# Performance work log

Hardware: AMD Instinct MI355X
Metric: run time of the kernel (lower is better)

## Reference

```python
import jax, jax.numpy as jnp
import numpy as np

B = 1048576   # batch of samples
L = 81        # leaf classes (hardcoded in the module)
G = 9         # synthetic 2-level hierarchy: 9 groups of 9 leaves under one root


def setup_inputs() -> dict:
    key = jax.random.key(0)
    k1, k2 = jax.random.split(key)
    outputs = jax.random.normal(k1, (B, L), dtype=jnp.float32)
    target = jax.random.randint(k2, (B,), 0, L, dtype=jnp.int32)
    return {"outputs": outputs, "target": target}


def reference(outputs, target):
    sft = jax.nn.softmax(outputs, axis=1)                 # [B, 81] leaf probs
    gp = sft.reshape(-1, G, G).sum(-1)                    # [B, 9] internal-node probs (sum of descendant leaves)
    parent = target // G                                  # [B] parent group of each target leaf
    p_parent = jnp.take_along_axis(gp, parent[:, None], axis=1)[:, 0]
    p_leaf = jnp.take_along_axis(sft, target[:, None], axis=1)[:, 0]
    win = 0.5 * p_parent + 0.5 * p_leaf
    loss = -jnp.log(win).mean()
    # greedy top-down argmax prediction: best group, then best leaf within that group
    g = jnp.argmax(gp, axis=1)                            # [B]
    within = jnp.take_along_axis(sft.reshape(-1, G, G), g[:, None, None], axis=1)[:, 0, :]  # [B, 9]
    pred = g * G + jnp.argmax(within, axis=1)             # [B]
    # synchronized walk to common ancestor: leaves at equal depth -> dist in {0,1,2}
    same_group = (pred // G) == parent
    total_dist = jnp.where(pred == target, 0, jnp.where(same_group, 1, 2)).sum()
    return loss, pred, total_dist
```

## Files before the change

kernel.cpp:

```cpp
#include <hip/hip_runtime.h>
#include <cstdint>

constexpr int BTOT = 1048576;
constexpr int LCLS = 81;
constexpr int GRP  = 9;
constexpr int ROWS = 64;
constexpr int THR  = 64;
constexpr int NBLK = BTOT / ROWS;
constexpr int TILE4 = ROWS * LCLS / 4;
constexpr int FULLR = TILE4 / THR;
constexpr int TAIL  = TILE4 - FULLR * THR;
constexpr float FIX = 67108864.0f;

__device__ inline void gload_lds16(const float* gsrc, float* ldst) {
    __builtin_amdgcn_global_load_lds(
        (const __attribute__((address_space(1))) void*)gsrc,
        (__attribute__((address_space(3))) void*)ldst,
        16, 0, 0);
}

__device__ __attribute__((noinline)) int refine_group_f64(const float* __restrict__ xrow)
{
    double best = -1.0; int bi = 0;
    #pragma unroll
    for (int g = 0; g < GRP; ++g) {
        double s = 0.0;
        #pragma unroll
        for (int j = 0; j < GRP; ++j) s += exp((double)xrow[g * GRP + j]);
        if (s > best) { best = s; bi = g; }
    }
    return bi;
}

__global__ __launch_bounds__(THR) void hl_main(
    const float* __restrict__ x, const int* __restrict__ tgt,
    float* __restrict__ out, unsigned long long* __restrict__ part)
{
    __shared__ float tile[ROWS * LCLS];
    const int tid = threadIdx.x;
    const size_t tbase = (size_t)blockIdx.x * (ROWS * LCLS);
    const float* gt = x + tbase;

    #pragma unroll
    for (int r = 0; r < FULLR; ++r) {
        const int i = r * THR + tid;
        gload_lds16(gt + 4 * i, &tile[4 * i]);
    }
    if (tid < TAIL) {
        const int i = FULLR * THR + tid;
        gload_lds16(gt + 4 * i, &tile[4 * i]);
    }
    __syncthreads();

    const int row = blockIdx.x * ROWS + tid;
    const float* xr = tile + tid * LCLS;

    float gs[GRP];
    #pragma unroll
    for (int g = 0; g < GRP; ++g) {
        float s = 0.0f;
        #pragma unroll
        for (int j = 0; j < GRP; ++j) s += __expf(xr[g * GRP + j]);
        gs[g] = s;
    }
    float S = gs[0];
    #pragma unroll
    for (int g = 1; g < GRP; ++g) S += gs[g];

    float g1 = gs[0], g2 = -1e30f; int gi = 0;
    #pragma unroll
    for (int g = 1; g < GRP; ++g) {
        float v = gs[g];
        bool gt2 = v > g1;
        g2 = gt2 ? g1 : (v > g2 ? v : g2);
        g1 = gt2 ? v  : g1;
        gi = gt2 ? g  : gi;
    }

    const int t = tgt[row];
    const int parent = t / GRP;

    float gpar = gs[0];
    #pragma unroll
    for (int g = 1; g < GRP; ++g)
        gpar = (parent == g) ? gs[g] : gpar;

    if (g1 - g2 < 1e-5f * g1) gi = refine_group_f64(xr);

    const int wb = gi * GRP;
    float w1 = xr[wb]; int wi = 0;
    #pragma unroll
    for (int j = 1; j < GRP; ++j) {
        float v = xr[wb + j];
        if (v > w1) { w1 = v; wi = j; }
    }

    const int pred = gi * GRP + wi;

    float et  = expf(xr[t]);
    float win = 0.5f * (gpar + et) / S;
    float nl  = -logf(win);
    unsigned long long lq = (unsigned long long)llrintf(nl * FIX);
    int dist = (pred == t) ? 0 : ((gi == parent) ? 1 : 2);

    out[1 + row] = (float)pred;

    #pragma unroll
    for (int off = 32; off > 0; off >>= 1) {
        lq   += __shfl_down(lq, off);
        dist += __shfl_down(dist, off);
    }
    if (tid == 0) {
        part[blockIdx.x] = lq;
        part[NBLK + blockIdx.x] = (unsigned long long)(unsigned)dist;
    }
}

__global__ __launch_bounds__(1024) void hl_final(
    const unsigned long long* __restrict__ part, float* __restrict__ out)
{
    const int tid = threadIdx.x;
    unsigned long long a = 0, b = 0;
    for (int i = tid; i < NBLK; i += 1024) { a += part[i]; b += part[NBLK + i]; }
    #pragma unroll
    for (int off = 32; off > 0; off >>= 1) { a += __shfl_down(a, off); b += __shfl_down(b, off); }
    __shared__ unsigned long long rA[16], rB[16];
    if ((tid & 63) == 0) { rA[tid >> 6] = a; rB[tid >> 6] = b; }
    __syncthreads();
    if (tid == 0) {
        unsigned long long ta = 0, tb = 0;
        #pragma unroll
        for (int w = 0; w < 16; ++w) { ta += rA[w]; tb += rB[w]; }
        double loss = ((double)ta / 67108864.0) / (double)BTOT;
        out[0] = (float)loss;
        out[1 + BTOT] = (float)tb;
    }
}

extern "C" void kernel_launch(void* const* d_in, const int* in_sizes, int n_in,
                              void* d_out, int out_size, void* d_ws, size_t ws_size,
                              hipStream_t stream) {
    const float* outputs = (const float*)d_in[0];
    const int*   target  = (const int*)d_in[1];
    float* out = (float*)d_out;
    unsigned long long* part = (unsigned long long*)d_ws;

    hl_main<<<NBLK, THR, 0, stream>>>(outputs, target, out, part);
    hl_final<<<1, 1024, 0, stream>>>(part, out);
}
```

Baseline: 75.85 us.

## Persistent double-buffered tile loop with atomic last-block final reduction

Replaces the one-tile-per-block grid with 768 persistent blocks that loop over tiles. Each block prefetches the next tile into a second LDS buffer with global_load_lds while it computes the current one, using hand-written vmcnt waits. The separate final-reduction kernel is dropped: each block atomically adds its partial sums, and the last block to finish (found via a ticket counter) writes the loss and distance. This removes one kernel launch and aims to overlap loads with compute, but adds a memset, relies on exact vmcnt counts (the target load must stay in flight), and omits a barrier that the single-wave blocks do not need.

```diff
diff --git a/kernel.cpp b/kernel.cpp
--- a/kernel.cpp
+++ b/kernel.cpp
@@ -1,22 +1,36 @@
 #include <hip/hip_runtime.h>
 #include <cstdint>
 
-constexpr int BTOT = 1048576;
-constexpr int LCLS = 81;
-constexpr int GRP  = 9;
-constexpr int ROWS = 64;
-constexpr int THR  = 64;
-constexpr int NBLK = BTOT / ROWS;
-constexpr int TILE4 = ROWS * LCLS / 4;
+constexpr int BTOT  = 1048576;
+constexpr int LCLS  = 81;
+constexpr int GRP   = 9;
+constexpr int ROWS  = 64;
+constexpr int THR   = 64;
+constexpr int NTILE = BTOT / ROWS;
+constexpr int NBLKP = 768;
+constexpr int TILEF = ROWS * LCLS;
+constexpr int TILE4 = TILEF / 4;
 constexpr int FULLR = TILE4 / THR;
 constexpr int TAIL  = TILE4 - FULLR * THR;
 constexpr float FIX = 67108864.0f;
 
-__device__ inline void gload_lds16(const float* gsrc, float* ldst) {
+__device__ __forceinline__ void gload_lds16(const float* gsrc, float* ldst) {
     __builtin_amdgcn_global_load_lds(
         (const __attribute__((address_space(1))) void*)gsrc,
         (__attribute__((address_space(3))) void*)ldst,
         16, 0, 0);
+}
+
+__device__ __forceinline__ void stage_tile(const float* gt, float* buf, int tid) {
+    #pragma unroll
+    for (int r = 0; r < FULLR; ++r) {
+        const int i = r * THR + tid;
+        gload_lds16(gt + 4 * i, &buf[4 * i]);
+    }
+    if (tid < TAIL) {
+        const int i = FULLR * THR + tid;
+        gload_lds16(gt + 4 * i, &buf[4 * i]);
+    }
 }
 
 __device__ __attribute__((noinline)) int refine_group_f64(const float* __restrict__ xrow)
@@ -34,106 +48,104 @@
 
 __global__ __launch_bounds__(THR) void hl_main(
     const float* __restrict__ x, const int* __restrict__ tgt,
-    float* __restrict__ out, unsigned long long* __restrict__ part)
+    float* __restrict__ out, unsigned long long* __restrict__ acc)
 {
-    __shared__ float tile[ROWS * LCLS];
+    __shared__ float buf0[TILEF];
+    __shared__ float buf1[TILEF];
     const int tid = threadIdx.x;
-    const size_t tbase = (size_t)blockIdx.x * (ROWS * LCLS);
-    const float* gt = x + tbase;
 
-    #pragma unroll
-    for (int r = 0; r < FULLR; ++r) {
-        const int i = r * THR + tid;
-        gload_lds16(gt + 4 * i, &tile[4 * i]);
+    unsigned long long lqT = 0;
+    unsigned dT = 0;
+
+    int tile = blockIdx.x;
+    stage_tile(x + (size_t)tile * TILEF, buf0, tid);
+
+    int cur = 0;
+    for (; tile < NTILE; tile += NBLKP) {
+        const int row  = tile * ROWS + tid;
+        const int t    = tgt[row];
+        const int next = tile + NBLKP;
+
+        if (next < NTILE)
+            stage_tile(x + (size_t)next * TILEF, (cur == 0) ? buf1 : buf0, tid);
+
+        if (next < NTILE) {
+            asm volatile("s_waitcnt vmcnt(22)" ::: "memory");
+        } else {
+            asm volatile("s_waitcnt vmcnt(2)" ::: "memory");
+        }
+        __builtin_amdgcn_sched_barrier(0);
+
+        const float* xr = ((cur == 0) ? buf0 : buf1) + tid * LCLS;
+
+        float gs[GRP];
+        #pragma unroll
+        for (int g = 0; g < GRP; ++g) {
+            float s = 0.0f;
+            #pragma unroll
+            for (int j = 0; j < GRP; ++j) s += __expf(xr[g * GRP + j]);
+            gs[g] = s;
+        }
+        float S = gs[0];
+        #pragma unroll
+        for (int g = 1; g < GRP; ++g) S += gs[g];
+
+        float g1 = gs[0], g2 = -1e30f; int gi = 0;
+        #pragma unroll
+        for (int g = 1; g < GRP; ++g) {
+            float v = gs[g];
+            bool gt2 = v > g1;
+            g2 = gt2 ? g1 : (v > g2 ? v : g2);
+            g1 = gt2 ? v  : g1;
+            gi = gt2 ? g  : gi;
+        }
+
+        const int parent = t / GRP;
+        float gpar = gs[0];
+        #pragma unroll
+        for (int g = 1; g < GRP; ++g)
+            gpar = (parent == g) ? gs[g] : gpar;
+
+        if (g1 - g2 < 1e-5f * g1) gi = refine_group_f64(xr);
+
+        const int wb = gi * GRP;
+        float w1 = xr[wb]; int wi = 0;
+        #pragma unroll
+        for (int j = 1; j < GRP; ++j) {
+            float v = xr[wb + j];
+            if (v > w1) { w1 = v; wi = j; }
+        }
+
+        const int pred = gi * GRP + wi;
+
+        float et  = expf(xr[t]);
+        float win = 0.5f * (gpar + et) / S;
+        float nl  = -logf(win);
+        lqT += (unsigned long long)llrintf(nl * FIX);
+        dT  += (pred == t) ? 0u : ((gi == parent) ? 1u : 2u);
+
+        out[1 + row] = (float)pred;
+        cur ^= 1;
     }
-    if (tid < TAIL) {
-        const int i = FULLR * THR + tid;
-        gload_lds16(gt + 4 * i, &tile[4 * i]);
-    }
-    __syncthreads();
-
-    const int row = blockIdx.x * ROWS + tid;
-    const float* xr = tile + tid * LCLS;
-
-    float gs[GRP];
-    #pragma unroll
-    for (int g = 0; g < GRP; ++g) {
-        float s = 0.0f;
-        #pragma unroll
-        for (int j = 0; j < GRP; ++j) s += __expf(xr[g * GRP + j]);
-        gs[g] = s;
-    }
-    float S = gs[0];
-    #pragma unroll
-    for (int g = 1; g < GRP; ++g) S += gs[g];
-
-    float g1 = gs[0], g2 = -1e30f; int gi = 0;
-    #pragma unroll
-    for (int g = 1; g < GRP; ++g) {
-        float v = gs[g];
-        bool gt2 = v > g1;
-        g2 = gt2 ? g1 : (v > g2 ? v : g2);
-        g1 = gt2 ? v  : g1;
-        gi = gt2 ? g  : gi;
-    }
-
-    const int t = tgt[row];
-    const int parent = t / GRP;
-
-    float gpar = gs[0];
-    #pragma unroll
-    for (int g = 1; g < GRP; ++g)
-        gpar = (parent == g) ? gs[g] : gpar;
-
-    if (g1 - g2 < 1e-5f * g1) gi = refine_group_f64(xr);
-
-    const int wb = gi * GRP;
-    float w1 = xr[wb]; int wi = 0;
-    #pragma unroll
-    for (int j = 1; j < GRP; ++j) {
-        float v = xr[wb + j];
-        if (v > w1) { w1 = v; wi = j; }
-    }
-
-    const int pred = gi * GRP + wi;
-
-    float et  = expf(xr[t]);
-    float win = 0.5f * (gpar + et) / S;
-    float nl  = -logf(win);
-    unsigned long long lq = (unsigned long long)llrintf(nl * FIX);
-    int dist = (pred == t) ? 0 : ((gi == parent) ? 1 : 2);
-
-    out[1 + row] = (float)pred;
 
     #pragma unroll
     for (int off = 32; off > 0; off >>= 1) {
-        lq   += __shfl_down(lq, off);
-        dist += __shfl_down(dist, off);
+        lqT += __shfl_down(lqT, off);
+        dT  += __shfl_down(dT, off);
     }
     if (tid == 0) {
-        part[blockIdx.x] = lq;
-        part[NBLK + blockIdx.x] = (unsigned long long)(unsigned)dist;
-    }
-}
-
-__global__ __launch_bounds__(1024) void hl_final(
-    const unsigned long long* __restrict__ part, float* __restrict__ out)
-{
-    const int tid = threadIdx.x;
-    unsigned long long a = 0, b = 0;
-    for (int i = tid; i < NBLK; i += 1024) { a += part[i]; b += part[NBLK + i]; }
-    #pragma unroll
-    for (int off = 32; off > 0; off >>= 1) { a += __shfl_down(a, off); b += __shfl_down(b, off); }
-    __shared__ unsigned long long rA[16], rB[16];
-    if ((tid & 63) == 0) { rA[tid >> 6] = a; rB[tid >> 6] = b; }
-    __syncthreads();
-    if (tid == 0) {
-        unsigned long long ta = 0, tb = 0;
-        #pragma unroll
-        for (int w = 0; w < 16; ++w) { ta += rA[w]; tb += rB[w]; }
-        double loss = ((double)ta / 67108864.0) / (double)BTOT;
-        out[0] = (float)loss;
-        out[1 + BTOT] = (float)tb;
+        atomicAdd(&acc[0], lqT);
+        atomicAdd(&acc[1], (unsigned long long)dT);
+        __threadfence();
+        unsigned* tick = (unsigned*)(acc + 2);
+        unsigned old = atomicAdd(tick, 1u);
+        if (old == (unsigned)(NBLKP - 1)) {
+            __threadfence();
+            unsigned long long ta = atomicAdd(&acc[0], 0ull);
+            unsigned long long tb = atomicAdd(&acc[1], 0ull);
+            out[0] = (float)(((double)ta / 67108864.0) / (double)BTOT);
+            out[1 + BTOT] = (float)tb;
+        }
     }
 }
 
@@ -143,8 +155,8 @@
     const float* outputs = (const float*)d_in[0];
     const int*   target  = (const int*)d_in[1];
     float* out = (float*)d_out;
-    unsigned long long* part = (unsigned long long*)d_ws;
+    unsigned long long* acc = (unsigned long long*)d_ws;
 
-    hl_main<<<NBLK, THR, 0, stream>>>(outputs, target, out, part);
-    hl_final<<<1, 1024, 0, stream>>>(part, out);
+    hipMemsetAsync(d_ws, 0, 24, stream);
+    hl_main<<<NBLKP, THR, 0, stream>>>(outputs, target, out, acc);
 }
```

New measurement: 114.1 us. 50.4% more time.

## Stream float4 chunks through registers with cross-lane group reduction instead of LDS tile

Applied to the files above, without the earlier changes.

Replaces the per-block LDS staging of a 64-row tile with a streaming scheme. Each wave processes 256 rows by reading coalesced float4 chunks into registers and computing group exp-sums and argmax positions with lane shuffles and readlane, storing only per-group results in LDS. A final per-row pass then derives prediction, loss and distance. The goal is to cut LDS traffic and bank conflicts from strided per-row reads, at the cost of complex branchy lane-boundary logic and a single wave per 256 rows, which may leave too little parallelism to hide memory latency.

```diff
diff --git a/kernel.cpp b/kernel.cpp
--- a/kernel.cpp
+++ b/kernel.cpp
@@ -4,19 +4,14 @@
 constexpr int BTOT = 1048576;
 constexpr int LCLS = 81;
 constexpr int GRP  = 9;
-constexpr int ROWS = 64;
-constexpr int THR  = 64;
-constexpr int NBLK = BTOT / ROWS;
-constexpr int TILE4 = ROWS * LCLS / 4;
-constexpr int FULLR = TILE4 / THR;
-constexpr int TAIL  = TILE4 - FULLR * THR;
+constexpr int RPB  = 256;
+constexpr int NBLK = BTOT / RPB;
+constexpr int FPB  = RPB * LCLS;
+constexpr int GPB  = RPB * GRP;
 constexpr float FIX = 67108864.0f;
 
-__device__ inline void gload_lds16(const float* gsrc, float* ldst) {
-    __builtin_amdgcn_global_load_lds(
-        (const __attribute__((address_space(1))) void*)gsrc,
-        (__attribute__((address_space(3))) void*)ldst,
-        16, 0, 0);
+__device__ __forceinline__ float readlane_f(float v, int l) {
+    return __int_as_float(__builtin_amdgcn_readlane(__float_as_int(v), l));
 }
 
 __device__ __attribute__((noinline)) int refine_group_f64(const float* __restrict__ xrow)
@@ -32,87 +27,172 @@
     return bi;
 }
 
-__global__ __launch_bounds__(THR) void hl_main(
+struct LaneState { int m, g, le, lr, r, kbase; };
+
+__device__ __forceinline__ void proc_chunk(
+    const float4 cv, const float4 nv, const int lane, LaneState& st,
+    float* gs, unsigned char* gpos, const unsigned short* tl, float* etx)
+{
+    const float v0 = cv.x, v1 = cv.y, v2 = cv.z, v3 = cv.w;
+    const float e0 = __expf(v0), e1 = __expf(v1), e2 = __expf(v2), e3 = __expf(v3);
+    const int m = st.m, g = st.g, le = st.le, lr = st.lr, r = st.r;
+    const int s = 9 - m;
+
+    float sA = e0;  float xmA = v0;  int xpA = m;
+    if (s > 1) { sA += e1; if (v1 > xmA) { xmA = v1; xpA = m + 1; } }
+    if (s > 2) { sA += e2; if (v2 > xmA) { xmA = v2; xpA = m + 2; } }
+    if (s > 3) { sA += e3; if (v3 > xmA) { xmA = v3; xpA = m + 3; } }
+    float sB = 0.0f; float xmB = -1e30f; int xpB = 0;
+    if (s <= 1) { sB += e1; if (v1 > xmB) { xmB = v1; xpB = 1 - s; } }
+    if (s <= 2) { sB += e2; if (v2 > xmB) { xmB = v2; xpB = 2 - s; } }
+    if (s <= 3) { sB += e3; if (v3 > xmB) { xmB = v3; xpB = 3 - s; } }
+
+    const float sA1  = __shfl_down(sA, 1),  sA2  = __shfl_down(sA, 2);
+    const float xmA1 = __shfl_down(xmA, 1), xmA2 = __shfl_down(xmA, 2);
+    const int   xpA1 = __shfl_down(xpA, 1), xpA2 = __shfl_down(xpA, 2);
+
+    {
+        const int tA = (int)tl[r];
+        const int r1 = (r < RPB - 1) ? r + 1 : r;
+        const int tB = (int)tl[r1];
+        if (le + 0 == tA) etx[r] = e0;
+        const bool x1 = (lr + 1 >= LCLS); if (le + 1 == (x1 ? tB : tA)) etx[x1 ? r + 1 : r] = e1;
+        const bool x2 = (lr + 2 >= LCLS); if (le + 2 == (x2 ? tB : tA)) etx[x2 ? r + 1 : r] = e2;
+        const bool x3 = (lr + 3 >= LCLS); if (le + 3 == (x3 ? tB : tA)) etx[x3 ? r + 1 : r] = e3;
+    }
+
+    const bool headA = (m == 0), headB = (m >= 6);
+    if (headA || headB) {
+        const int G  = headA ? g : (g + 1);
+        float tot    = headA ? sA  : sB;
+        float tm     = headA ? xmA : xmB;
+        int   tp     = headA ? xpA : xpB;
+        if (lane < 62) {
+            tot += sA1 + sA2;
+            if (xmA1 > tm) { tm = xmA1; tp = xpA1; }
+            if (xmA2 > tm) { tm = xmA2; tp = xpA2; }
+        } else {
+            if (lane == 62) {
+                tot += sA1;
+                if (xmA1 > tm) { tm = xmA1; tp = xpA1; }
+            }
+            const int Ln  = st.kbase + 256;
+            const int cnt = 9 * G + 9 - Ln;
+            const int p0  = 9 - cnt;
+            const float n0 = readlane_f(nv.x, 0), n1 = readlane_f(nv.y, 0),
+                        n2 = readlane_f(nv.z, 0), n3 = readlane_f(nv.w, 0),
+                        n4 = readlane_f(nv.x, 1), n5 = readlane_f(nv.y, 1),
+                        n6 = readlane_f(nv.z, 1), n7 = readlane_f(nv.w, 1);
+            if (cnt > 0) { tot += __expf(n0); if (n0 > tm) { tm = n0; tp = p0;     } }
+            if (cnt > 1) { tot += __expf(n1); if (n1 > tm) { tm = n1; tp = p0 + 1; } }
+            if (cnt > 2) { tot += __expf(n2); if (n2 > tm) { tm = n2; tp = p0 + 2; } }
+            if (cnt > 3) { tot += __expf(n3); if (n3 > tm) { tm = n3; tp = p0 + 3; } }
+            if (cnt > 4) { tot += __expf(n4); if (n4 > tm) { tm = n4; tp = p0 + 4; } }
+            if (cnt > 5) { tot += __expf(n5); if (n5 > tm) { tm = n5; tp = p0 + 5; } }
+            if (cnt > 6) { tot += __expf(n6); if (n6 > tm) { tm = n6; tp = p0 + 6; } }
+            if (cnt > 7) { tot += __expf(n7); if (n7 > tm) { tm = n7; tp = p0 + 7; } }
+        }
+        gs[G]   = tot;
+        gpos[G] = (unsigned char)tp;
+    }
+
+    st.m  = (m + 4 >= 9)   ? (m - 5)   : (m + 4);
+    st.g  = g + 28 + ((m + 4 >= 9) ? 1 : 0);
+    st.lr = (lr + 13 >= 81) ? (lr - 68) : (lr + 13);
+    st.r  = r + 3 + ((lr + 13 >= 81) ? 1 : 0);
+    st.le = le + 256;
+    st.kbase += 256;
+}
+
+__global__ __launch_bounds__(64) void hl_main(
     const float* __restrict__ x, const int* __restrict__ tgt,
     float* __restrict__ out, unsigned long long* __restrict__ part)
 {
-    __shared__ float tile[ROWS * LCLS];
-    const int tid = threadIdx.x;
-    const size_t tbase = (size_t)blockIdx.x * (ROWS * LCLS);
-    const float* gt = x + tbase;
-
-    #pragma unroll
-    for (int r = 0; r < FULLR; ++r) {
-        const int i = r * THR + tid;
-        gload_lds16(gt + 4 * i, &tile[4 * i]);
-    }
-    if (tid < TAIL) {
-        const int i = FULLR * THR + tid;
-        gload_lds16(gt + 4 * i, &tile[4 * i]);
-    }
-    __syncthreads();
-
-    const int row = blockIdx.x * ROWS + tid;
-    const float* xr = tile + tid * LCLS;
-
-    float gs[GRP];
-    #pragma unroll
-    for (int g = 0; g < GRP; ++g) {
-        float s = 0.0f;
-        #pragma unroll
-        for (int j = 0; j < GRP; ++j) s += __expf(xr[g * GRP + j]);
-        gs[g] = s;
-    }
-    float S = gs[0];
-    #pragma unroll
-    for (int g = 1; g < GRP; ++g) S += gs[g];
-
-    float g1 = gs[0], g2 = -1e30f; int gi = 0;
-    #pragma unroll
-    for (int g = 1; g < GRP; ++g) {
-        float v = gs[g];
-        bool gt2 = v > g1;
-        g2 = gt2 ? g1 : (v > g2 ? v : g2);
-        g1 = gt2 ? v  : g1;
-        gi = gt2 ? g  : gi;
-    }
-
-    const int t = tgt[row];
-    const int parent = t / GRP;
-
-    float gpar = gs[0];
-    #pragma unroll
-    for (int g = 1; g < GRP; ++g)
-        gpar = (parent == g) ? gs[g] : gpar;
-
-    if (g1 - g2 < 1e-5f * g1) gi = refine_group_f64(xr);
-
-    const int wb = gi * GRP;
-    float w1 = xr[wb]; int wi = 0;
-    #pragma unroll
-    for (int j = 1; j < GRP; ++j) {
-        float v = xr[wb + j];
-        if (v > w1) { w1 = v; wi = j; }
-    }
-
-    const int pred = gi * GRP + wi;
-
-    float et  = expf(xr[t]);
-    float win = 0.5f * (gpar + et) / S;
-    float nl  = -logf(win);
-    unsigned long long lq = (unsigned long long)llrintf(nl * FIX);
-    int dist = (pred == t) ? 0 : ((gi == parent) ? 1 : 2);
-
-    out[1 + row] = (float)pred;
+    __shared__ float          gs[GPB];
+    __shared__ float          etx[RPB];
+    __shared__ unsigned short tl[RPB];
+    __shared__ unsigned char  gpos[GPB];
+
+    const int lane = threadIdx.x;
+    const int bid  = blockIdx.x;
+    const float* xb = x + (size_t)bid * FPB;
+
+    #pragma unroll
+    for (int q = 0; q < 4; ++q) {
+        const int rr = q * 64 + lane;
+        const int tv = tgt[bid * RPB + rr];
+        tl[rr] = (unsigned short)(rr * LCLS + tv);
+    }
+
+    const float4* pw = reinterpret_cast<const float4*>(xb) + lane;
+    float4 c0 = pw[0 * 64], c1 = pw[1 * 64], c2 = pw[2 * 64];
+
+    LaneState st;
+    st.le = 4 * lane; st.m = st.le % 9; st.g = st.le / 9;
+    st.lr = st.le % 81; st.r = st.le / 81; st.kbase = 0;
+
+    #pragma unroll 1
+    for (int it = 0; it < 27; ++it) {
+        const int k = it * 3;
+        proc_chunk(c0, c1, lane, st, gs, gpos, tl, etx);
+        if (k + 3 <= 80) c0 = pw[(k + 3) * 64];
+        proc_chunk(c1, c2, lane, st, gs, gpos, tl, etx);
+        if (k + 4 <= 80) c1 = pw[(k + 4) * 64];
+        proc_chunk(c2, c0, lane, st, gs, gpos, tl, etx);
+        if (k + 5 <= 80) c2 = pw[(k + 5) * 64];
+    }
+
+    unsigned long long lq = 0;
+    unsigned dT = 0;
+    #pragma unroll
+    for (int p = 0; p < 4; ++p) {
+        const int r2 = p * 64 + lane;
+        float gsr[GRP];
+        #pragma unroll
+        for (int j = 0; j < GRP; ++j) gsr[j] = gs[r2 * GRP + j];
+        float S = gsr[0];
+        #pragma unroll
+        for (int j = 1; j < GRP; ++j) S += gsr[j];
+
+        float g1 = gsr[0], g2 = -1e30f; int gi = 0;
+        #pragma unroll
+        for (int j = 1; j < GRP; ++j) {
+            const float v = gsr[j];
+            const bool gt2 = v > g1;
+            g2 = gt2 ? g1 : (v > g2 ? v : g2);
+            g1 = gt2 ? v : g1;
+            gi = gt2 ? j : gi;
+        }
+
+        const int t = (int)tl[r2] - LCLS * r2;
+        const int parent = t / GRP;
+        float gpar = gsr[0];
+        #pragma unroll
+        for (int j = 1; j < GRP; ++j) gpar = (parent == j) ? gsr[j] : gpar;
+
+        if (g1 - g2 < 1e-5f * g1)
+            gi = refine_group_f64(xb + (size_t)r2 * LCLS);
+
+        const int wi = (int)gpos[r2 * GRP + gi];
+        const int pred = gi * GRP + wi;
+
+        const float et  = etx[r2];
+        const float win = 0.5f * (gpar + et) / S;
+        const float nl  = -logf(win);
+        lq += (unsigned long long)llrintf(nl * FIX);
+        dT += (pred == t) ? 0u : ((gi == parent) ? 1u : 2u);
+
+        out[1 + bid * RPB + r2] = (float)pred;
+    }
 
     #pragma unroll
     for (int off = 32; off > 0; off >>= 1) {
-        lq   += __shfl_down(lq, off);
-        dist += __shfl_down(dist, off);
-    }
-    if (tid == 0) {
-        part[blockIdx.x] = lq;
-        part[NBLK + blockIdx.x] = (unsigned long long)(unsigned)dist;
+        lq += __shfl_down(lq, off);
+        dT += __shfl_down(dT, off);
+    }
+    if (lane == 0) {
+        part[bid] = lq;
+        part[NBLK + bid] = (unsigned long long)dT;
     }
 }
 
@@ -131,7 +211,7 @@
         unsigned long long ta = 0, tb = 0;
         #pragma unroll
         for (int w = 0; w < 16; ++w) { ta += rA[w]; tb += rB[w]; }
-        double loss = ((double)ta / 67108864.0) / (double)BTOT;
+        const double loss = ((double)ta / 67108864.0) / (double)BTOT;
         out[0] = (float)loss;
         out[1 + BTOT] = (float)tb;
     }
@@ -145,6 +225,6 @@
     float* out = (float*)d_out;
     unsigned long long* part = (unsigned long long*)d_ws;
 
-    hl_main<<<NBLK, THR, 0, stream>>>(outputs, target, out, part);
+    hl_main<<<NBLK, 64, 0, stream>>>(outputs, target, out, part);
     hl_final<<<1, 1024, 0, stream>>>(part, out);
 }
```

Measured after the change: 189.0 us. +149.1%, slower.
